# Performance work log

Hardware: AMD Instinct MI355X
Metric: run time of the kernel (lower is better)

The kernel has to match this reference:

```python
import jax, jax.numpy as jnp
import numpy as np

EPS = 1e-6

def setup_inputs() -> dict:
    key = jax.random.key(0)
    k1, k2, k3, k4, k5 = jax.random.split(key, 5)
    B, Lq, Lk, D, Dc = 8, 1024, 8192, 256, 128
    q = jax.random.normal(k1, (B, Lq, D), dtype=jnp.float32)
    k_q = jax.random.randint(k2, (B, Lk, Dc), 0, 16, dtype=jnp.int32)  # 4-bit codes
    k_scale = jax.random.uniform(k3, (B, 1, Dc), dtype=jnp.float32)
    k_zero = jax.random.uniform(k4, (B, 1, Dc), dtype=jnp.float32) * 15.0
    W_up = jax.random.normal(k5, (D, Dc), dtype=jnp.float32) / np.sqrt(Dc)
    return {"q": q, "k_q": k_q, "k_scale": k_scale, "k_zero": k_zero, "W_up": W_up}

def reference(q, k_q, k_scale, k_zero, W_up):
    # int4 dequantization: (B, Lk, Dc)
    k_c = k_scale * (k_q.astype(jnp.float32) - k_zero)
    # low-rank decompress (nn.Linear(d_compressed, d_model, bias=False)): k = k_c @ W_up.T -> (B, Lk, D)
    k = jnp.einsum('blc,dc->bld', k_c, W_up)
    # squared norms (raw values used in diff, clamped values used in denominator)
    q_sq = jnp.sum(q * q, axis=-1)  # (B, Lq)
    k_sq = jnp.sum(k * k, axis=-1)  # (B, Lk)
    q_norm_sq = jnp.minimum(q_sq, 1.0 - EPS)
    k_norm_sq = jnp.minimum(k_sq, 1.0 - EPS)
    # ||q_i - k_j||^2 via expansion (same math as materializing the diff tensor)
    qk = jnp.einsum('bqd,bkd->bqk', q, k)  # (B, Lq, Lk)
    diff_norm_sq = jnp.maximum(q_sq[:, :, None] + k_sq[:, None, :] - 2.0 * qk, 0.0)
    denom = (1.0 - q_norm_sq)[:, :, None] * (1.0 - k_norm_sq)[:, None, :] + EPS
    dist = jnp.arccosh(1.0 + 2.0 * diff_norm_sq / denom)  # (B, Lq, Lk)
    return dist
```

## Files before the change

kernel.cpp:

```cpp
#include <hip/hip_runtime.h>
#include <hip/hip_bf16.h>

#define B_   8
#define LQ   1024
#define LK   8192
#define D_   256
#define DC   128
#define EPSF 1e-6f

typedef __attribute__((ext_vector_type(8))) short short8;
typedef __attribute__((ext_vector_type(4))) float floatx4;

static __device__ __forceinline__ floatx4 mfma16(short8 a, short8 b, floatx4 c) {
    return __builtin_amdgcn_mfma_f32_16x16x32_bf16(a, b, c, 0, 0, 0);
}
static __device__ __forceinline__ float fast_rcp(float x)  { return __builtin_amdgcn_rcpf(x); }
static __device__ __forceinline__ float fast_sqrt(float x) { return __builtin_amdgcn_sqrtf(x); }
static __device__ __forceinline__ float fast_ln(float x)   { return 0.69314718056f * __builtin_amdgcn_logf(x); }

__global__ __launch_bounds__(512) void k_G(const float* __restrict__ W,
                                           __hip_bfloat16* __restrict__ G,
                                           __hip_bfloat16* __restrict__ Wt) {
    __shared__ float red[512];
    int c1 = blockIdx.x;
    int t = threadIdx.x, c2 = t & 127, h = t >> 7;
    int d0 = h * 64;
    float a0 = 0.f, a1 = 0.f, a2 = 0.f, a3 = 0.f;
#pragma unroll 4
    for (int d = 0; d < 64; d += 4) {
        a0 += W[(size_t)(d0 + d + 0) * DC + c1] * W[(size_t)(d0 + d + 0) * DC + c2];
        a1 += W[(size_t)(d0 + d + 1) * DC + c1] * W[(size_t)(d0 + d + 1) * DC + c2];
        a2 += W[(size_t)(d0 + d + 2) * DC + c1] * W[(size_t)(d0 + d + 2) * DC + c2];
        a3 += W[(size_t)(d0 + d + 3) * DC + c1] * W[(size_t)(d0 + d + 3) * DC + c2];
    }
    red[t] = (a0 + a1) + (a2 + a3);
    if (t < 256) Wt[(size_t)c1 * D_ + t] = __float2bfloat16(W[(size_t)t * DC + c1]);
    __syncthreads();
    if (h == 0)
        G[c1 * DC + c2] =
            __float2bfloat16(red[c2] + red[128 + c2] + red[256 + c2] + red[384 + c2]);
}

__global__ __launch_bounds__(256) void k_qproj(const float* __restrict__ q,
                                               const __hip_bfloat16* __restrict__ Wt,
                                               __hip_bfloat16* __restrict__ qproj,
                                               float* __restrict__ q_sq) {
    __shared__ __hip_bfloat16 sA[32 * 72];
    __shared__ __hip_bfloat16 sB[128 * 72];
    int t = threadIdx.x, lane = t & 63, w = t >> 6;
    int quad = lane >> 4, li = lane & 15;
    int wm = w >> 1, wn = w & 1;
    int row0 = blockIdx.x * 32;

    float psum[2] = {0.f, 0.f};
    floatx4 acc[4];
#pragma unroll
    for (int nt = 0; nt < 4; ++nt) acc[nt] = (floatx4){0.f, 0.f, 0.f, 0.f};

    for (int kc4 = 0; kc4 < 4; ++kc4) {
#pragma unroll
        for (int it = 0; it < 2; ++it) {
            int idx = it * 256 + t;
            int r = idx >> 4, pos = idx & 15;
            float4 v = *(const float4*)(q + (size_t)(row0 + r) * D_ + kc4 * 64 + pos * 4);
            psum[it] += v.x * v.x + v.y * v.y + v.z * v.z + v.w * v.w;
            __hip_bfloat16* dst = &sA[r * 72 + pos * 4];
            dst[0] = __float2bfloat16(v.x); dst[1] = __float2bfloat16(v.y);
            dst[2] = __float2bfloat16(v.z); dst[3] = __float2bfloat16(v.w);
        }
#pragma unroll
        for (int it = 0; it < 4; ++it) {
            int e = it * 256 + t;
            int c = e >> 3, ch = e & 7;
            *(uint4*)&sB[c * 72 + ch * 8] =
                *(const uint4*)(Wt + (size_t)c * D_ + kc4 * 64 + ch * 8);
        }
        __syncthreads();
        short8 af[2];
#pragma unroll
        for (int ks = 0; ks < 2; ++ks)
            af[ks] = *(const short8*)&sA[(wm * 16 + li) * 72 + ks * 32 + quad * 8];
#pragma unroll
        for (int nt = 0; nt < 4; ++nt)
#pragma unroll
            for (int ks = 0; ks < 2; ++ks) {
                short8 bf = *(const short8*)&sB[((wn * 4 + nt) * 16 + li) * 72 + ks * 32 + quad * 8];
                acc[nt] = mfma16(af[ks], bf, acc[nt]);
            }
        __syncthreads();
    }
#pragma unroll
    for (int nt = 0; nt < 4; ++nt)
#pragma unroll
        for (int r = 0; r < 4; ++r) {
            int row = wm * 16 + quad * 4 + r;
            qproj[(size_t)(row0 + row) * DC + (wn * 4 + nt) * 16 + li] =
                __float2bfloat16(acc[nt][r]);
        }
#pragma unroll
    for (int it = 0; it < 2; ++it) {
        float s = psum[it];
        s += __shfl_xor(s, 1); s += __shfl_xor(s, 2);
        s += __shfl_xor(s, 4); s += __shfl_xor(s, 8);
        if (li == 0) q_sq[row0 + it * 16 + w * 4 + quad] = s;
    }
}

__global__ __launch_bounds__(256) void k_dq_ksq(const int* __restrict__ kq,
                                                const float* __restrict__ kscale,
                                                const float* __restrict__ kzero,
                                                const __hip_bfloat16* __restrict__ G,
                                                __hip_bfloat16* __restrict__ kc,
                                                float* __restrict__ k_sq) {
    __shared__ __hip_bfloat16 sK[64 * 132];
    int t = threadIdx.x, lane = t & 63, w = t >> 6;
    int quad = lane >> 4, li = lane & 15;
    int b = blockIdx.x >> 7, l0 = (blockIdx.x & 127) * 64;

    const int4* codes = (const int4*)(kq + ((size_t)b * LK + l0) * DC);
    int col = (t & 31) * 4;
    float4 sc = *(const float4*)(kscale + b * DC + col);
    float4 zp = *(const float4*)(kzero + b * DC + col);
    __hip_bfloat16* kco = kc + ((size_t)b * LK + l0) * DC;
#pragma unroll
    for (int it = 0; it < 8; ++it) {
        int idx = it * 256 + t;
        int r = idx >> 5;
        int4 c4 = codes[idx];
        __hip_bfloat16 tmp[4];
        tmp[0] = __float2bfloat16(sc.x * ((float)c4.x - zp.x));
        tmp[1] = __float2bfloat16(sc.y * ((float)c4.y - zp.y));
        tmp[2] = __float2bfloat16(sc.z * ((float)c4.z - zp.z));
        tmp[3] = __float2bfloat16(sc.w * ((float)c4.w - zp.w));
        *(uint2*)&sK[r * 132 + col] = *(const uint2*)tmp;
        *(uint2*)(kco + idx * 4)    = *(const uint2*)tmp;
    }
    __syncthreads();

    short8 af[4];
#pragma unroll
    for (int ks = 0; ks < 4; ++ks)
        af[ks] = *(const short8*)&sK[(w * 16 + li) * 132 + ks * 32 + quad * 8];
    float s4[4] = {0.f, 0.f, 0.f, 0.f};
#pragma unroll
    for (int nt = 0; nt < 8; ++nt) {
        floatx4 a0 = (floatx4){0.f, 0.f, 0.f, 0.f};
#pragma unroll
        for (int ks = 0; ks < 4; ++ks) {
            short8 bf = *(const short8*)(G + (size_t)(nt * 16 + li) * DC + ks * 32 + quad * 8);
            a0 = mfma16(af[ks], bf, a0);
        }
        int c2 = nt * 16 + li;
#pragma unroll
        for (int r = 0; r < 4; ++r)
            s4[r] += a0[r] * __bfloat162float(sK[(w * 16 + quad * 4 + r) * 132 + c2]);
    }
#pragma unroll
    for (int r = 0; r < 4; ++r) {
        float v = s4[r];
        v += __shfl_xor(v, 1); v += __shfl_xor(v, 2);
        v += __shfl_xor(v, 4); v += __shfl_xor(v, 8);
        if (li == 0)
            k_sq[(size_t)b * LK + l0 + w * 16 + quad * 4 + r] = v;
    }
}

__global__ __launch_bounds__(256) void k_main(const __hip_bfloat16* __restrict__ qproj,
                                              const __hip_bfloat16* __restrict__ kc,
                                              const float* __restrict__ q_sq,
                                              const float* __restrict__ k_sq,
                                              float* __restrict__ out) {
    __shared__ __align__(16) char smem[128 * 72 * 2 * 2];
    __hip_bfloat16* sA = (__hip_bfloat16*)smem;
    __hip_bfloat16* sB = sA + 128 * 72;
    float* sO = (float*)smem;

    int t = threadIdx.x, lane = t & 63, w = t >> 6;
    int quad = lane >> 4, li = lane & 15;
    int wm = w >> 1, wn = w & 1;
    int bid = blockIdx.x;
    int b   = bid & 7;
    int rem = bid >> 3;
    int m0  = (rem & 7) << 7;
    int n0  = (rem >> 3) << 7;
    const uint4* Ag = (const uint4*)(qproj + ((size_t)b * LQ + m0) * DC);
    const uint4* Bg = (const uint4*)(kc   + ((size_t)b * LK + n0) * DC);
    uint4* dA = (uint4*)sA; uint4* dB = (uint4*)sB;

    floatx4 acc[4][4];
#pragma unroll
    for (int i = 0; i < 4; ++i)
#pragma unroll
        for (int j = 0; j < 4; ++j)
            acc[i][j] = (floatx4){0.f, 0.f, 0.f, 0.f};

    int r_ = t >> 3, ch_ = t & 7;
    uint4 ra[4], rb[4];
#pragma unroll
    for (int it = 0; it < 4; ++it) {
        ra[it] = Ag[(it * 32 + r_) * 16 + ch_];
        rb[it] = Bg[(it * 32 + r_) * 16 + ch_];
    }
#pragma unroll
    for (int it = 0; it < 4; ++it) {
        dA[(it * 32 + r_) * 9 + ch_] = ra[it];
        dB[(it * 32 + r_) * 9 + ch_] = rb[it];
    }
    __syncthreads();
#pragma unroll
    for (int it = 0; it < 4; ++it) {
        ra[it] = Ag[(it * 32 + r_) * 16 + 8 + ch_];
        rb[it] = Bg[(it * 32 + r_) * 16 + 8 + ch_];
    }
#pragma unroll
    for (int ks = 0; ks < 2; ++ks) {
        short8 qf[4], kf[4];
#pragma unroll
        for (int i = 0; i < 4; ++i) {
            qf[i] = *(const short8*)&sA[(wm * 64 + i * 16 + li) * 72 + ks * 32 + quad * 8];
            kf[i] = *(const short8*)&sB[(wn * 64 + i * 16 + li) * 72 + ks * 32 + quad * 8];
        }
#pragma unroll
        for (int i = 0; i < 4; ++i)
#pragma unroll
            for (int j = 0; j < 4; ++j)
                acc[i][j] = mfma16(kf[j], qf[i], acc[i][j]);
    }
    __syncthreads();
#pragma unroll
    for (int it = 0; it < 4; ++it) {
        dA[(it * 32 + r_) * 9 + ch_] = ra[it];
        dB[(it * 32 + r_) * 9 + ch_] = rb[it];
    }
    __syncthreads();
#pragma unroll
    for (int ks = 0; ks < 2; ++ks) {
        short8 qf[4], kf[4];
#pragma unroll
        for (int i = 0; i < 4; ++i) {
            qf[i] = *(const short8*)&sA[(wm * 64 + i * 16 + li) * 72 + ks * 32 + quad * 8];
            kf[i] = *(const short8*)&sB[(wn * 64 + i * 16 + li) * 72 + ks * 32 + quad * 8];
        }
#pragma unroll
        for (int i = 0; i < 4; ++i)
#pragma unroll
            for (int j = 0; j < 4; ++j)
                acc[i][j] = mfma16(kf[j], qf[i], acc[i][j]);
    }

    int orow_t = t >> 4;
    int ocol4  = (t & 15) * 4;
    float qsA[8], omqA[8];
#pragma unroll
    for (int qq = 0; qq < 8; ++qq) {
        qsA[qq]  = q_sq[(size_t)b * LQ + m0 + qq * 16 + orow_t];
        omqA[qq] = 1.f - fminf(qsA[qq], 1.f - EPSF);
    }
#pragma unroll
    for (int p = 0; p < 2; ++p) {
        __syncthreads();
#pragma unroll
        for (int jj = 0; jj < 2; ++jj) {
            int c = wn * 32 + jj * 16 + quad * 4;
#pragma unroll
            for (int i = 0; i < 4; ++i) {
                int m = wm * 64 + i * 16 + li;
                *(floatx4*)&sO[m * 68 + c] = acc[i][p * 2 + jj];
            }
        }
        __syncthreads();
        int nbase = (ocol4 >> 5) * 64 + p * 32 + (ocol4 & 31);
        floatx4 ks4 = *(const floatx4*)(k_sq + (size_t)b * LK + n0 + nbase);
        floatx4 kn;
#pragma unroll
        for (int r = 0; r < 4; ++r)
            kn[r] = 1.f - fminf(ks4[r], 1.f - EPSF);
#pragma unroll
        for (int qq = 0; qq < 8; ++qq) {
            int row = qq * 16 + orow_t;
            floatx4 v = *(const floatx4*)&sO[row * 68 + ocol4];
            float qs = qsA[qq], omq = omqA[qq];
            floatx4 o;
#pragma unroll
            for (int r = 0; r < 4; ++r) {
                float diff  = fmaxf(qs + ks4[r] - 2.f * v[r], 0.f);
                float delta = 2.f * diff * fast_rcp(omq * kn[r] + EPSF);
                float sq    = fast_sqrt(delta * (delta + 2.f));
                o[r] = fast_ln(1.f + delta + sq);
            }
            __builtin_nontemporal_store(
                o, (floatx4*)(out + ((size_t)b * LQ + m0 + row) * (size_t)LK + n0 + nbase));
        }
    }
}

extern "C" void kernel_launch(void* const* d_in, const int* in_sizes, int n_in,
                              void* d_out, int out_size, void* d_ws, size_t ws_size,
                              hipStream_t stream) {
    const float* q      = (const float*)d_in[0];
    const int*   kq     = (const int*)d_in[1];
    const float* kscale = (const float*)d_in[2];
    const float* kzero  = (const float*)d_in[3];
    const float* W      = (const float*)d_in[4];
    float* out = (float*)d_out;

    char* ws = (char*)d_ws;
    __hip_bfloat16* qproj = (__hip_bfloat16*)(ws);
    __hip_bfloat16* kc    = (__hip_bfloat16*)(ws + 2097152);
    __hip_bfloat16* G     = (__hip_bfloat16*)(ws + 18874368);
    float*          q_sq  = (float*)(ws + 18907136);
    float*          k_sq  = (float*)(ws + 18939904);
    __hip_bfloat16* Wt    = kc;

    k_G     <<<128, 512, 0, stream>>>(W, G, Wt);
    k_qproj <<<256, 256, 0, stream>>>(q, Wt, qproj, q_sq);
    k_dq_ksq<<<1024, 256, 0, stream>>>(kq, kscale, kzero, G, kc, k_sq);
    k_main  <<<4096, 256, 0, stream>>>(qproj, kc, q_sq, k_sq, out);
}
```

Baseline: 388.9 us.

## Load GEMM tiles directly to LDS with XOR swizzle and store outputs from registers

Replaces the register-staged global-to-LDS tile copies with global_load_lds direct transfers into an XOR-swizzled, unpadded LDS layout. The epilogue no longer transposes accumulators through shared memory and writes 16-byte output chunks straight from the MFMA accumulator layout. Launch bounds now request 4 blocks per CU. This removes the LDS round trip and several barriers, but drops the explicit double-buffer prefetch overlap and gives output stores less coalescing (64-byte row segments per quad instead of full contiguous rows).

```diff
diff --git a/kernel.cpp b/kernel.cpp
--- a/kernel.cpp
+++ b/kernel.cpp
@@ -17,6 +17,12 @@
 static __device__ __forceinline__ float fast_rcp(float x)  { return __builtin_amdgcn_rcpf(x); }
 static __device__ __forceinline__ float fast_sqrt(float x) { return __builtin_amdgcn_sqrtf(x); }
 static __device__ __forceinline__ float fast_ln(float x)   { return 0.69314718056f * __builtin_amdgcn_logf(x); }
+
+static __device__ __forceinline__ void gl16(const void* g, void* l) {
+    __builtin_amdgcn_global_load_lds(
+        (const __attribute__((address_space(1))) unsigned int*)g,
+        (__attribute__((address_space(3))) unsigned int*)l, 16, 0, 0);
+}
 
 __global__ __launch_bounds__(512) void k_G(const float* __restrict__ W,
                                            __hip_bfloat16* __restrict__ G,
@@ -165,16 +171,13 @@
     }
 }
 
-__global__ __launch_bounds__(256) void k_main(const __hip_bfloat16* __restrict__ qproj,
-                                              const __hip_bfloat16* __restrict__ kc,
-                                              const float* __restrict__ q_sq,
-                                              const float* __restrict__ k_sq,
-                                              float* __restrict__ out) {
-    __shared__ __align__(16) char smem[128 * 72 * 2 * 2];
-    __hip_bfloat16* sA = (__hip_bfloat16*)smem;
-    __hip_bfloat16* sB = sA + 128 * 72;
-    float* sO = (float*)smem;
-
+__global__ __launch_bounds__(256, 4) void k_main(const __hip_bfloat16* __restrict__ qproj,
+                                                 const __hip_bfloat16* __restrict__ kc,
+                                                 const float* __restrict__ q_sq,
+                                                 const float* __restrict__ k_sq,
+                                                 float* __restrict__ out) {
+    __shared__ __hip_bfloat16 sA[128 * 64];
+    __shared__ __hip_bfloat16 sB[128 * 64];
     int t = threadIdx.x, lane = t & 63, w = t >> 6;
     int quad = lane >> 4, li = lane & 15;
     int wm = w >> 1, wn = w & 1;
@@ -183,9 +186,11 @@
     int rem = bid >> 3;
     int m0  = (rem & 7) << 7;
     int n0  = (rem >> 3) << 7;
-    const uint4* Ag = (const uint4*)(qproj + ((size_t)b * LQ + m0) * DC);
-    const uint4* Bg = (const uint4*)(kc   + ((size_t)b * LK + n0) * DC);
-    uint4* dA = (uint4*)sA; uint4* dB = (uint4*)sB;
+    const char* Ag = (const char*)(qproj + ((size_t)b * LQ + m0) * DC);
+    const char* Bg = (const char*)(kc   + ((size_t)b * LK + n0) * DC);
+
+    int lrow = lane >> 3;
+    int lch  = (lane & 7) ^ lrow;
 
     floatx4 acc[4][4];
 #pragma unroll
@@ -194,102 +199,59 @@
         for (int j = 0; j < 4; ++j)
             acc[i][j] = (floatx4){0.f, 0.f, 0.f, 0.f};
 
-    int r_ = t >> 3, ch_ = t & 7;
-    uint4 ra[4], rb[4];
-#pragma unroll
-    for (int it = 0; it < 4; ++it) {
-        ra[it] = Ag[(it * 32 + r_) * 16 + ch_];
-        rb[it] = Bg[(it * 32 + r_) * 16 + ch_];
-    }
-#pragma unroll
-    for (int it = 0; it < 4; ++it) {
-        dA[(it * 32 + r_) * 9 + ch_] = ra[it];
-        dB[(it * 32 + r_) * 9 + ch_] = rb[it];
-    }
-    __syncthreads();
-#pragma unroll
-    for (int it = 0; it < 4; ++it) {
-        ra[it] = Ag[(it * 32 + r_) * 16 + 8 + ch_];
-        rb[it] = Bg[(it * 32 + r_) * 16 + 8 + ch_];
-    }
-#pragma unroll
-    for (int ks = 0; ks < 2; ++ks) {
-        short8 qf[4], kf[4];
-#pragma unroll
-        for (int i = 0; i < 4; ++i) {
-            qf[i] = *(const short8*)&sA[(wm * 64 + i * 16 + li) * 72 + ks * 32 + quad * 8];
-            kf[i] = *(const short8*)&sB[(wn * 64 + i * 16 + li) * 72 + ks * 32 + quad * 8];
-        }
-#pragma unroll
-        for (int i = 0; i < 4; ++i)
-#pragma unroll
-            for (int j = 0; j < 4; ++j)
-                acc[i][j] = mfma16(kf[j], qf[i], acc[i][j]);
-    }
-    __syncthreads();
-#pragma unroll
-    for (int it = 0; it < 4; ++it) {
-        dA[(it * 32 + r_) * 9 + ch_] = ra[it];
-        dB[(it * 32 + r_) * 9 + ch_] = rb[it];
-    }
-    __syncthreads();
-#pragma unroll
-    for (int ks = 0; ks < 2; ++ks) {
-        short8 qf[4], kf[4];
-#pragma unroll
-        for (int i = 0; i < 4; ++i) {
-            qf[i] = *(const short8*)&sA[(wm * 64 + i * 16 + li) * 72 + ks * 32 + quad * 8];
-            kf[i] = *(const short8*)&sB[(wn * 64 + i * 16 + li) * 72 + ks * 32 + quad * 8];
-        }
-#pragma unroll
-        for (int i = 0; i < 4; ++i)
-#pragma unroll
-            for (int j = 0; j < 4; ++j)
-                acc[i][j] = mfma16(kf[j], qf[i], acc[i][j]);
-    }
-
-    int orow_t = t >> 4;
-    int ocol4  = (t & 15) * 4;
-    float qsA[8], omqA[8];
-#pragma unroll
-    for (int qq = 0; qq < 8; ++qq) {
-        qsA[qq]  = q_sq[(size_t)b * LQ + m0 + qq * 16 + orow_t];
-        omqA[qq] = 1.f - fminf(qsA[qq], 1.f - EPSF);
-    }
-#pragma unroll
-    for (int p = 0; p < 2; ++p) {
+#pragma unroll
+    for (int h = 0; h < 2; ++h) {
+#pragma unroll
+        for (int it = 0; it < 4; ++it) {
+            int rbase = it * 32 + w * 8;
+            size_t goff = (size_t)(rbase + lrow) * 256 + (size_t)(h * 8 + lch) * 16;
+            gl16(Ag + goff, (char*)sA + rbase * 128);
+            gl16(Bg + goff, (char*)sB + rbase * 128);
+        }
         __syncthreads();
 #pragma unroll
-        for (int jj = 0; jj < 2; ++jj) {
-            int c = wn * 32 + jj * 16 + quad * 4;
+        for (int ks = 0; ks < 2; ++ks) {
+            int ac = ((ks * 4 + quad) ^ (li & 7)) * 16;
+            short8 qf[4], kf[4];
 #pragma unroll
             for (int i = 0; i < 4; ++i) {
-                int m = wm * 64 + i * 16 + li;
-                *(floatx4*)&sO[m * 68 + c] = acc[i][p * 2 + jj];
+                qf[i] = *(const short8*)((const char*)sA + (wm * 64 + i * 16 + li) * 128 + ac);
+                kf[i] = *(const short8*)((const char*)sB + (wn * 64 + i * 16 + li) * 128 + ac);
             }
-        }
-        __syncthreads();
-        int nbase = (ocol4 >> 5) * 64 + p * 32 + (ocol4 & 31);
-        floatx4 ks4 = *(const floatx4*)(k_sq + (size_t)b * LK + n0 + nbase);
-        floatx4 kn;
+#pragma unroll
+            for (int i = 0; i < 4; ++i)
+#pragma unroll
+                for (int j = 0; j < 4; ++j)
+                    acc[i][j] = mfma16(kf[j], qf[i], acc[i][j]);
+        }
+        if (h == 0) __syncthreads();
+    }
+
+    floatx4 ks4[4], kn4[4];
+#pragma unroll
+    for (int j = 0; j < 4; ++j) {
+        ks4[j] = *(const floatx4*)(k_sq + (size_t)b * LK + n0 + wn * 64 + j * 16 + quad * 4);
 #pragma unroll
         for (int r = 0; r < 4; ++r)
-            kn[r] = 1.f - fminf(ks4[r], 1.f - EPSF);
-#pragma unroll
-        for (int qq = 0; qq < 8; ++qq) {
-            int row = qq * 16 + orow_t;
-            floatx4 v = *(const floatx4*)&sO[row * 68 + ocol4];
-            float qs = qsA[qq], omq = omqA[qq];
+            kn4[j][r] = 1.f - fminf(ks4[j][r], 1.f - EPSF);
+    }
+#pragma unroll
+    for (int i = 0; i < 4; ++i) {
+        int m = m0 + wm * 64 + i * 16 + li;
+        float qs  = q_sq[(size_t)b * LQ + m];
+        float omq = 1.f - fminf(qs, 1.f - EPSF);
+        float* orow = out + ((size_t)b * LQ + m) * (size_t)LK + n0 + wn * 64;
+#pragma unroll
+        for (int j = 0; j < 4; ++j) {
             floatx4 o;
 #pragma unroll
             for (int r = 0; r < 4; ++r) {
-                float diff  = fmaxf(qs + ks4[r] - 2.f * v[r], 0.f);
-                float delta = 2.f * diff * fast_rcp(omq * kn[r] + EPSF);
+                float diff  = fmaxf(qs + ks4[j][r] - 2.f * acc[i][j][r], 0.f);
+                float delta = 2.f * diff * fast_rcp(omq * kn4[j][r] + EPSF);
                 float sq    = fast_sqrt(delta * (delta + 2.f));
                 o[r] = fast_ln(1.f + delta + sq);
             }
-            __builtin_nontemporal_store(
-                o, (floatx4*)(out + ((size_t)b * LQ + m0 + row) * (size_t)LK + n0 + nbase));
+            __builtin_nontemporal_store(o, (floatx4*)(orow + j * 16 + quad * 4));
         }
     }
 }
```

After: 357.1 us. 1.09x faster.
